# Kernel optimization log

Hardware: AMD Instinct MI355X
Metric: run time of the kernel (lower is better)

The kernel has to match this reference:

```python
import jax, jax.numpy as jnp
import numpy as np

R = 7          # region_size
BW = 2.5       # KDE bandwidth
EPS = 1e-8

def _blur5x5(x):
    # AvgPool2d(kernel=5, stride=1, padding=2, count_include_pad=True)
    s = jax.lax.reduce_window(x, 0.0, jax.lax.add, (1, 1, 5, 5), (1, 1, 1, 1),
                              [(0, 0), (0, 0), (2, 2), (2, 2)])
    return s / 25.0

def setup_inputs() -> dict:
    key = jax.random.key(0)
    x = jax.random.uniform(key, (2, 2, 1, 80, 80), dtype=jnp.float32) * 255.0
    return {"x": x}

def reference(x):
    N, SF, C, H, W = x.shape
    B = N * SF
    xi = x.reshape(B, C, H, W)

    # unsharp-mask style preprocessing (round/clamp as in torch)
    smooth = jnp.round(_blur5x5(xi))
    sharp = jnp.round(jnp.clip(2.5 * xi - 1.25 * smooth, 0.0, 255.0))
    division = jnp.round(jnp.clip(sharp * 255.0 / (smooth + EPS), 0.0, 255.0))

    Hp, Wp = H - R + 1, W - R + 1
    L = R * R
    # overlapping RxR patches: (B, C*R*R, Hp, Wp), features ordered (C, R, R)
    patches = jax.lax.conv_general_dilated_patches(division, (R, R), (1, 1), 'VALID')
    patches = patches.reshape(B, C, L, Hp * Wp).transpose(0, 3, 2, 1)  # (B, P, L, C)

    # KDE-based local entropy: p_i = mean_j N(x_i - x_j; 0, BW^2 I_C)
    d2 = jnp.sum((patches[:, :, :, None, :] - patches[:, :, None, :, :]) ** 2, axis=-1)  # (B,P,L,L)
    inv2b2 = 1.0 / (2.0 * BW * BW)
    norm = (2.0 * np.pi * BW * BW) ** (C / 2.0)
    p = jnp.exp(-d2 * inv2b2).mean(axis=-1) / norm          # (B, P, L)
    ent = -jnp.mean(jnp.log(p + EPS), axis=-1)              # (B, P)

    ent = ent.reshape(B, Hp, Wp)
    pad = R // 2
    ent = jnp.pad(ent, ((0, 0), (pad, pad), (pad, pad)))    # back to (B, H, W)
    return ent.reshape(N, SF, H, W)
```

## Files before the change

### kernel.cpp

```cpp
#include <hip/hip_runtime.h>
#include <math.h>

#define BATCH 4
#define H 80
#define W 80
#define R 7
#define HP 74
#define L 49
#define PAD 3

__device__ __forceinline__ float clamp255(float v) {
    return fminf(fmaxf(v, 0.0f), 255.0f);
}

__global__ void preprocess_kernel(const float* __restrict__ x, float* __restrict__ divimg) {
    int idx = blockIdx.x * blockDim.x + threadIdx.x;
    if (idx >= BATCH * H * W) return;
    int b  = idx / (H * W);
    int r  = idx % (H * W);
    int y  = r / W;
    int xc = r % W;
    const float* img = x + b * H * W;

    double s = 0.0;
    #pragma unroll
    for (int dy = -2; dy <= 2; ++dy) {
        int yy = y + dy;
        if (yy < 0 || yy >= H) continue;
        #pragma unroll
        for (int dx = -2; dx <= 2; ++dx) {
            int xx = xc + dx;
            if (xx < 0 || xx >= W) continue;
            s += (double)img[yy * W + xx];
        }
    }
    float smooth = rintf((float)(s / 25.0));
    float xv = img[y * W + xc];
    float sharp = rintf(clamp255(__fsub_rn(__fmul_rn(2.5f, xv), __fmul_rn(1.25f, smooth))));
    float dv = rintf(clamp255(__fdiv_rn(__fmul_rn(sharp, 255.0f), __fadd_rn(smooth, 1e-8f))));
    divimg[idx] = dv;
}

__global__ void entropy_kernel(const float* __restrict__ divimg, float* __restrict__ out) {
    const float KSCALE = 0.33972871239731236f;
    const float PSCALE = 1.0f / (49.0f * 6.266570686577501f);
    const float EPS    = 1e-8f;
    const float LN2_49 = 0.6931471805599453f / 49.0f;

    int gtid = blockIdx.x * blockDim.x + threadIdx.x;
    int wave = gtid >> 6;
    int lane = threadIdx.x & 63;
    if (wave >= BATCH * H * W) return;

    int b  = wave / (H * W);
    int r  = wave % (H * W);
    int oy = r / W;
    int ox = r % W;

    if (oy < PAD || oy >= H - PAD || ox < PAD || ox >= W - PAD) {
        if (lane == 0) out[wave] = 0.0f;
        return;
    }
    int py = oy - PAD;
    int px = ox - PAD;

    float u = 0.0f;
    if (lane < L) {
        int rr = lane / R;
        int cc = lane - rr * R;
        u = divimg[b * H * W + (py + rr) * W + (px + cc)] * KSCALE;
    }

    float acc = 0.0f;
    #pragma unroll
    for (int j = 0; j < L; ++j) {
        float uj = __uint_as_float(__builtin_amdgcn_readlane(__float_as_uint(u), j));
        float s  = u - uj;
        acc += __builtin_amdgcn_exp2f(-(s * s));
    }

    float t = 0.0f;
    if (lane < L) {
        t = __builtin_amdgcn_logf(fmaf(acc, PSCALE, EPS));
    }
    #pragma unroll
    for (int off = 32; off; off >>= 1) {
        t += __shfl_xor(t, off, 64);
    }
    if (lane == 0) {
        out[wave] = -t * LN2_49;
    }
}

extern "C" void kernel_launch(void* const* d_in, const int* in_sizes, int n_in,
                              void* d_out, int out_size, void* d_ws, size_t ws_size,
                              hipStream_t stream) {
    const float* x = (const float*)d_in[0];
    float* out = (float*)d_out;
    float* divimg = (float*)d_ws;

    preprocess_kernel<<<(BATCH * H * W + 255) / 256, 256, 0, stream>>>(x, divimg);

    entropy_kernel<<<(BATCH * H * W * 64 + 255) / 256, 256, 0, stream>>>(divimg, out);
}
```

Measured before the change: 72.65 us.

## Compute 2x2 output tile per wave using shared 8x8 pixel window

Each wave now loads an 8x8 window of the preprocessed image and computes the pairwise Gaussian kernel once. It then accumulates four masked sums covering the four overlapping 7x7 patches of a 2x2 output tile. This cuts the number of waves by four and reuses each exp2 evaluation across up to four outputs, at the cost of 64 exp evaluations instead of 49 and four accumulators plus four reductions. Border outputs are written as zero through clamped loads and validity masks.

```diff
diff --git a/kernel.cpp b/kernel.cpp
--- a/kernel.cpp
+++ b/kernel.cpp
@@ -5,9 +5,10 @@
 #define H 80
 #define W 80
 #define R 7
-#define HP 74
 #define L 49
 #define PAD 3
+#define TILES_X 40
+#define TILES 1600
 
 __device__ __forceinline__ float clamp255(float v) {
     return fminf(fmaxf(v, 0.0f), 255.0f);
@@ -50,45 +51,60 @@
     int gtid = blockIdx.x * blockDim.x + threadIdx.x;
     int wave = gtid >> 6;
     int lane = threadIdx.x & 63;
-    if (wave >= BATCH * H * W) return;
+    if (wave >= BATCH * TILES) return;
 
-    int b  = wave / (H * W);
-    int r  = wave % (H * W);
-    int oy = r / W;
-    int ox = r % W;
+    int b   = wave / TILES;
+    int rem = wave % TILES;
+    int ty  = rem / TILES_X;
+    int tx  = rem % TILES_X;
+    int oy0 = 2 * ty;
+    int ox0 = 2 * tx;
 
-    if (oy < PAD || oy >= H - PAD || ox < PAD || ox >= W - PAD) {
-        if (lane == 0) out[wave] = 0.0f;
-        return;
-    }
-    int py = oy - PAD;
-    int px = ox - PAD;
+    int lr = lane >> 3;
+    int lc = lane & 7;
+    int iy = oy0 - PAD + lr;  iy = iy < 0 ? 0 : (iy > H - 1 ? H - 1 : iy);
+    int ix = ox0 - PAD + lc;  ix = ix < 0 ? 0 : (ix > W - 1 ? W - 1 : ix);
+    float u = divimg[b * H * W + iy * W + ix] * KSCALE;
 
-    float u = 0.0f;
-    if (lane < L) {
-        int rr = lane / R;
-        int cc = lane - rr * R;
-        u = divimg[b * H * W + (py + rr) * W + (px + cc)] * KSCALE;
+    float a00 = 0.0f, a01 = 0.0f, a10 = 0.0f, a11 = 0.0f;
+    #pragma unroll
+    for (int j = 0; j < 64; ++j) {
+        float uj = __uint_as_float(__builtin_amdgcn_readlane(__float_as_uint(u), j));
+        float s  = u - uj;
+        float e  = __builtin_amdgcn_exp2f(-(s * s));
+        int rj = j >> 3, cj = j & 7;
+        if (rj < 7 && cj < 7) a00 += e;
+        if (rj < 7 && cj >= 1) a01 += e;
+        if (rj >= 1 && cj < 7) a10 += e;
+        if (rj >= 1 && cj >= 1) a11 += e;
     }
 
-    float acc = 0.0f;
+    float t00 = (lr < 7 && lc < 7) ? __builtin_amdgcn_logf(fmaf(a00, PSCALE, EPS)) : 0.0f;
+    float t01 = (lr < 7 && lc >= 1) ? __builtin_amdgcn_logf(fmaf(a01, PSCALE, EPS)) : 0.0f;
+    float t10 = (lr >= 1 && lc < 7) ? __builtin_amdgcn_logf(fmaf(a10, PSCALE, EPS)) : 0.0f;
+    float t11 = (lr >= 1 && lc >= 1) ? __builtin_amdgcn_logf(fmaf(a11, PSCALE, EPS)) : 0.0f;
     #pragma unroll
-    for (int j = 0; j < L; ++j) {
-        float uj = __uint_as_float(__builtin_amdgcn_readlane(__float_as_uint(u), j));
-        float s  = u - uj;
-        acc += __builtin_amdgcn_exp2f(-(s * s));
+    for (int off = 32; off; off >>= 1) {
+        t00 += __shfl_xor(t00, off, 64);
+        t01 += __shfl_xor(t01, off, 64);
+        t10 += __shfl_xor(t10, off, 64);
+        t11 += __shfl_xor(t11, off, 64);
     }
 
-    float t = 0.0f;
-    if (lane < L) {
-        t = __builtin_amdgcn_logf(fmaf(acc, PSCALE, EPS));
-    }
-    #pragma unroll
-    for (int off = 32; off; off >>= 1) {
-        t += __shfl_xor(t, off, 64);
-    }
     if (lane == 0) {
-        out[wave] = -t * LN2_49;
+        float* outb = out + b * H * W;
+        int oy1 = oy0 + 1, ox1 = ox0 + 1;
+        bool iy0ok = (oy0 >= PAD) && (oy0 < H - PAD);
+        bool iy1ok = (oy1 >= PAD) && (oy1 < H - PAD);
+        bool ix0ok = (ox0 >= PAD) && (ox0 < W - PAD);
+        bool ix1ok = (ox1 >= PAD) && (ox1 < W - PAD);
+        float2 row0, row1;
+        row0.x = (iy0ok && ix0ok) ? -t00 * LN2_49 : 0.0f;
+        row0.y = (iy0ok && ix1ok) ? -t01 * LN2_49 : 0.0f;
+        row1.x = (iy1ok && ix0ok) ? -t10 * LN2_49 : 0.0f;
+        row1.y = (iy1ok && ix1ok) ? -t11 * LN2_49 : 0.0f;
+        *(float2*)(outb + oy0 * W + ox0) = row0;
+        *(float2*)(outb + oy1 * W + ox0) = row1;
     }
 }
 
@@ -101,5 +117,5 @@
 
     preprocess_kernel<<<(BATCH * H * W + 255) / 256, 256, 0, stream>>>(x, divimg);
 
-    entropy_kernel<<<(BATCH * H * W * 64 + 255) / 256, 256, 0, stream>>>(divimg, out);
+    entropy_kernel<<<(BATCH * TILES * 64 + 255) / 256, 256, 0, stream>>>(divimg, out);
 }
```

New measurement: 66.92 us. -7.9%, faster.
